# Kernel tuning notes

Measured on AMD Instinct MI355X. Metric: run time of the kernel, lower is better.

The kernel has to match this reference:

```python
import jax, jax.numpy as jnp
import numpy as np

K = 3
STRIDE = 1
PAD = 1
DIL = 1


def conv2d(x, w, b, stride, pad, dil):
    y = jax.lax.conv_general_dilated(
        x, w, (stride, stride), [(pad, pad), (pad, pad)],
        rhs_dilation=(dil, dil), dimension_numbers=("NCHW", "OIHW", "NCHW"))
    return y + b[None, :, None, None]


def bilinear_gather(img, ys, xs):
    # img: (C,H,W); ys,xs: (KK,Ho,Wo) pixel coords.
    # grid_sample(mode=bilinear, padding_mode=zeros, align_corners=True):
    # out-of-range corners contribute 0, interpolation weights unchanged.
    H, W = img.shape[-2:]
    y0 = jnp.floor(ys)
    x0 = jnp.floor(xs)
    wy1 = ys - y0
    wx1 = xs - x0
    wy0 = 1.0 - wy1
    wx0 = 1.0 - wx1

    def g(yc, xc):
        yi = yc.astype(jnp.int32)
        xi = xc.astype(jnp.int32)
        valid = (yi >= 0) & (yi < H) & (xi >= 0) & (xi < W)
        yi = jnp.clip(yi, 0, H - 1)
        xi = jnp.clip(xi, 0, W - 1)
        v = img[:, yi, xi]  # (C,KK,Ho,Wo)
        return v * valid[None].astype(img.dtype)

    return (g(y0, x0) * (wy0 * wx0)[None]
            + g(y0, x0 + 1.0) * (wy0 * wx1)[None]
            + g(y0 + 1.0, x0) * (wy1 * wx0)[None]
            + g(y0 + 1.0, x0 + 1.0) * (wy1 * wx1)[None])


def setup_inputs() -> dict:
    key = jax.random.key(0)
    ks = jax.random.split(key, 4)
    B, C_in, H, W = 8, 64, 96, 96
    C_out = 64
    x = jax.random.normal(ks[0], (B, C_in, H, W), dtype=jnp.float32)
    weight = jax.random.normal(ks[1], (C_out, C_in, K, K), dtype=jnp.float32) * 0.05
    bias = jax.random.normal(ks[2], (C_out,), dtype=jnp.float32) * 0.01
    off_w = jax.random.normal(ks[3], (2 * K * K, C_in, K, K), dtype=jnp.float32) * 0.05
    off_b = jnp.zeros((2 * K * K,), dtype=jnp.float32)
    return {"x": x, "weight": weight, "bias": bias, "off_w": off_w, "off_b": off_b}


def reference(x, weight, bias, off_w, off_b):
    B, C, H, W = x.shape
    Ho = (H + 2 * PAD - DIL * (K - 1) - 1) // STRIDE + 1
    Wo = (W + 2 * PAD - DIL * (K - 1) - 1) // STRIDE + 1

    offsets = conv2d(x, off_w, off_b, STRIDE, PAD, DIL)  # (B,2*K*K,Ho,Wo)
    off = offsets.reshape(B, K * K, 2, Ho, Wo)

    # Base sampling grid (note: original code does NOT subtract padding; kept faithful).
    by, bx = jnp.meshgrid(jnp.arange(Ho, dtype=x.dtype), jnp.arange(Wo, dtype=x.dtype), indexing="ij")
    by = by * STRIDE + (K // 2) * DIL
    bx = bx * STRIDE + (K // 2) * DIL
    ko = jnp.arange(-(K // 2), K // 2 + 1, dtype=x.dtype)
    ky, kx = jnp.meshgrid(ko, ko, indexing="ij")

    sy = by[None, None] + ky.reshape(1, -1, 1, 1) + off[:, :, 0]  # (B,KK,Ho,Wo)
    sx = bx[None, None] + kx.reshape(1, -1, 1, 1) + off[:, :, 1]

    sampled = jax.vmap(bilinear_gather)(x, sy, sx)  # (B,C,KK,Ho,Wo)

    wflat = weight.reshape(weight.shape[0], C, K * K)  # (O,C,KK)
    out = jnp.einsum("bckhw,ock->bohw", sampled, wflat)
    return out + bias[None, :, None, None]
```

## Files before the change

### kernel.cpp

```cpp
#include <hip/hip_runtime.h>

#define HH 96
#define WW 96
#define HW 9216
#define NB 8

typedef __bf16 bf16x8 __attribute__((ext_vector_type(8)));
typedef float  f32x4  __attribute__((ext_vector_type(4)));

union BF8 { uint4 u; bf16x8 v; unsigned short s[8]; };

__device__ __forceinline__ unsigned short f2bf_bits(float f) {
    unsigned u = __float_as_uint(f);
    unsigned r = u + 0x7FFFu + ((u >> 16) & 1u);
    return (unsigned short)(r >> 16);
}
__device__ __forceinline__ float bf2f(unsigned short s) {
    return __uint_as_float(((unsigned)s) << 16);
}

__device__ __forceinline__ void bl_setup(int h, int w, int r, int s, float oy, float ox,
                                         int* a, float* wg) {
    float sy = (float)(h + r) + oy;
    float sx = (float)(w + s) + ox;
    float fy = floorf(sy), fx = floorf(sx);
    int   y0 = (int)fy, x0 = (int)fx;
    int   y1 = y0 + 1, x1 = x0 + 1;
    float wy1 = sy - fy, wx1 = sx - fx;
    float wy0 = 1.f - wy1, wx0 = 1.f - wx1;
    float m00 = (y0 >= 0 && y0 < HH && x0 >= 0 && x0 < WW) ? 1.f : 0.f;
    float m01 = (y0 >= 0 && y0 < HH && x1 >= 0 && x1 < WW) ? 1.f : 0.f;
    float m10 = (y1 >= 0 && y1 < HH && x0 >= 0 && x0 < WW) ? 1.f : 0.f;
    float m11 = (y1 >= 0 && y1 < HH && x1 >= 0 && x1 < WW) ? 1.f : 0.f;
    int cy0 = min(max(y0, 0), HH - 1), cy1 = min(max(y1, 0), HH - 1);
    int cx0 = min(max(x0, 0), WW - 1), cx1 = min(max(x1, 0), WW - 1);
    a[0] = (cy0 * WW + cx0) * 64;  a[1] = (cy0 * WW + cx1) * 64;
    a[2] = (cy1 * WW + cx0) * 64;  a[3] = (cy1 * WW + cx1) * 64;
    wg[0] = wy0 * wx0 * m00;  wg[1] = wy0 * wx1 * m01;
    wg[2] = wy1 * wx0 * m10;  wg[3] = wy1 * wx1 * m11;
}

__global__ __launch_bounds__(256) void xcvt_prep(const float* __restrict__ x,
                                                 const float* __restrict__ weight,
                                                 const float* __restrict__ off_w,
                                                 unsigned short* __restrict__ xt,
                                                 unsigned short* __restrict__ wTb,
                                                 unsigned short* __restrict__ owTb) {
    __shared__ unsigned short T[64 * 64];
    int bid   = blockIdx.x;
    int t     = threadIdx.x;
    int b     = bid & 7;
    int pbase = (bid >> 3) * 64;
    int pl    = t & 63;
    int q     = t >> 6;

    const float* xp = x + ((size_t)(b * 64 + q * 16)) * HW + pbase + pl;
    unsigned short hb[16];
#pragma unroll
    for (int i = 0; i < 16; ++i) hb[i] = f2bf_bits(xp[(size_t)i * HW]);

    uint4 w0, w1;
    w0.x = hb[0]  | (hb[1]  << 16); w0.y = hb[2]  | (hb[3]  << 16);
    w0.z = hb[4]  | (hb[5]  << 16); w0.w = hb[6]  | (hb[7]  << 16);
    w1.x = hb[8]  | (hb[9]  << 16); w1.y = hb[10] | (hb[11] << 16);
    w1.z = hb[12] | (hb[13] << 16); w1.w = hb[14] | (hb[15] << 16);
    int sw = pl & 7;
    *(uint4*)&T[pl * 64 + (((2 * q)     ^ sw) << 3)] = w0;
    *(uint4*)&T[pl * 64 + (((2 * q + 1) ^ sw) << 3)] = w1;
    __syncthreads();

    int row = t >> 2, rs = row & 7;
    uint4 a  = *(const uint4*)&T[row * 64 + ((((t & 3) * 2)     ^ rs) << 3)];
    uint4 b2 = *(const uint4*)&T[row * 64 + ((((t & 3) * 2 + 1) ^ rs) << 3)];
    unsigned short* dst = xt + ((size_t)(b * HW + pbase)) * 64 + t * 16;
    *(uint4*)dst       = a;
    *(uint4*)(dst + 8) = b2;

    if (bid < 216) {
        int i = bid * 256 + t;
        if (i < 36864) {
            int tap = i >> 12;
            int co  = (i >> 6) & 63;
            int c   = i & 63;
            wTb[i] = f2bf_bits(weight[(co * 64 + c) * 9 + tap]);
        } else {
            int f   = i - 36864;
            int j   = f / 576;
            int kk  = f - j * 576;
            int tap = kk >> 6;
            int c   = kk & 63;
            owTb[f] = (j < 18) ? f2bf_bits(off_w[(j * 64 + c) * 9 + tap]) : (unsigned short)0;
        }
    }
}

__global__ __launch_bounds__(256) void offs_mfma(const unsigned short* __restrict__ xt,
                                                 const unsigned short* __restrict__ owTb,
                                                 const float* __restrict__ ob,
                                                 float* __restrict__ off) {
    __shared__ unsigned short S[64 * 64];

    int bid   = blockIdx.x;
    int t     = threadIdx.x;
    int b     = bid & 7;
    int pbase = (bid >> 3) * 64;

    int e    = t & 7;
    int base = t >> 3;
    int px0  = pbase + base;
    int px1  = px0 + 32;
    int h0 = px0 / WW, w0 = px0 - h0 * WW;
    int h1 = px1 / WW, w1 = px1 - h1 * WW;
    int sw = base & 7;

    int ln = t & 15;
    int qd = (t >> 4) & 3;
    int pt = t >> 6;

    f32x4 accj[2] = {{0.f, 0.f, 0.f, 0.f}, {0.f, 0.f, 0.f, 0.f}};
    const unsigned short* xb = xt + (size_t)b * HW * 64;

    for (int tap = 0; tap < 9; ++tap) {
        int r = tap / 3, s = tap - r * 3;

        int  iy0 = h0 - 1 + r, ix0 = w0 - 1 + s;
        bool v0  = (iy0 >= 0) & (iy0 < HH) & (ix0 >= 0) & (ix0 < WW);
        int  a0  = (min(max(iy0, 0), HH - 1) * WW + min(max(ix0, 0), WW - 1)) * 64;
        int  iy1 = h1 - 1 + r, ix1 = w1 - 1 + s;
        bool v1  = (iy1 >= 0) & (iy1 < HH) & (ix1 >= 0) & (ix1 < WW);
        int  a1  = (min(max(iy1, 0), HH - 1) * WW + min(max(ix1, 0), WW - 1)) * 64;

        uint4 p0 = *(const uint4*)(xb + a0 + e * 8);
        uint4 p1 = *(const uint4*)(xb + a1 + e * 8);
        if (!v0) p0 = make_uint4(0, 0, 0, 0);
        if (!v1) p1 = make_uint4(0, 0, 0, 0);
        *(uint4*)&S[base * 64 + ((e ^ sw) << 3)]        = p0;
        *(uint4*)&S[(base + 32) * 64 + ((e ^ sw) << 3)] = p1;
        __syncthreads();

        int  row = pt * 16 + ln, rs = row & 7;
        BF8  fa0, fa1;
        fa0.u = *(const uint4*)&S[row * 64 + ((qd       ^ rs) << 3)];
        fa1.u = *(const uint4*)&S[row * 64 + (((qd + 4) ^ rs) << 3)];
#pragma unroll
        for (int jt = 0; jt < 2; ++jt) {
            const unsigned short* brow = owTb + (size_t)(jt * 16 + ln) * 576 + tap * 64 + qd * 8;
            BF8 fb0, fb1;
            fb0.u = *(const uint4*)brow;
            fb1.u = *(const uint4*)(brow + 32);
            accj[jt] = __builtin_amdgcn_mfma_f32_16x16x32_bf16(fa0.v, fb0.v, accj[jt], 0, 0, 0);
            accj[jt] = __builtin_amdgcn_mfma_f32_16x16x32_bf16(fa1.v, fb1.v, accj[jt], 0, 0, 0);
        }
        __syncthreads();
    }

    int pxo = pbase + pt * 16 + qd * 4;
    {
        float bv = ob[ln];
        float4 st;
        st.x = accj[0].x + bv; st.y = accj[0].y + bv;
        st.z = accj[0].z + bv; st.w = accj[0].w + bv;
        *(float4*)(off + ((size_t)(b * 18 + ln)) * HW + pxo) = st;
    }
    if (ln < 2) {
        int   j  = 16 + ln;
        float bv = ob[j];
        float4 st;
        st.x = accj[1].x + bv; st.y = accj[1].y + bv;
        st.z = accj[1].z + bv; st.w = accj[1].w + bv;
        *(float4*)(off + ((size_t)(b * 18 + j)) * HW + pxo) = st;
    }
}

__global__ __launch_bounds__(256) void deform_main(const unsigned short* __restrict__ xt,
                                                   const unsigned short* __restrict__ wTb,
                                                   const float* __restrict__ bias,
                                                   const float* __restrict__ off,
                                                   float* __restrict__ out) {
    __shared__ unsigned short S[64 * 64];
    __shared__ unsigned short Wk[64 * 64];

    int bid   = blockIdx.x;
    int t     = threadIdx.x;
    int b     = bid & 7;
    int pbase = (bid >> 3) * 64;

    int e    = t & 7;
    int base = t >> 3;
    int px0  = pbase + base;
    int px1  = px0 + 32;
    int h0 = px0 / WW, w0 = px0 - h0 * WW;
    int h1 = px1 / WW, w1 = px1 - h1 * WW;
    int sw = base & 7;

    int ln = t & 15;
    int qd = (t >> 4) & 3;
    int ct = t >> 6;

    const unsigned short* xb = xt + (size_t)b * HW * 64;
    const float* offb = off + (size_t)b * 18 * HW;

    f32x4 acc[4] = {{0.f,0.f,0.f,0.f},{0.f,0.f,0.f,0.f},{0.f,0.f,0.f,0.f},{0.f,0.f,0.f,0.f}};

    float oy0 = offb[0 * HW + px0], ox0 = offb[1 * HW + px0];
    float oy1 = offb[0 * HW + px1], ox1 = offb[1 * HW + px1];

    for (int tap = 0; tap < 9; ++tap) {
        int r = tap / 3, s = tap - r * 3;

        int   a0[4], a1[4];
        float g0[4], g1[4];
        bl_setup(h0, w0, r, s, oy0, ox0, a0, g0);
        bl_setup(h1, w1, r, s, oy1, ox1, a1, g1);

        uint4 cA[4], cB[4];
#pragma unroll
        for (int c = 0; c < 4; ++c) cA[c] = *(const uint4*)(xb + a0[c] + e * 8);
#pragma unroll
        for (int c = 0; c < 4; ++c) cB[c] = *(const uint4*)(xb + a1[c] + e * 8);

        float oy0N = 0.f, ox0N = 0.f, oy1N = 0.f, ox1N = 0.f;
        if (tap < 8) {
            oy0N = offb[(2 * tap + 2) * HW + px0]; ox0N = offb[(2 * tap + 3) * HW + px0];
            oy1N = offb[(2 * tap + 2) * HW + px1]; ox1N = offb[(2 * tap + 3) * HW + px1];
        }

        {
            const uint4* wsrc = (const uint4*)(wTb + (size_t)tap * 4096);
            uint4 wa = wsrc[2 * t];
            uint4 wb = wsrc[2 * t + 1];
            int co = t >> 2, cs = co & 7;
            int c0 = (t & 3) * 2;
            *(uint4*)&Wk[co * 64 + ((c0       ^ cs) << 3)] = wa;
            *(uint4*)&Wk[co * 64 + (((c0 + 1) ^ cs) << 3)] = wb;
        }

        {
            BF8 q0, q1, q2, q3;
            q0.u = cA[0]; q1.u = cA[1]; q2.u = cA[2]; q3.u = cA[3];
            unsigned short ov[8];
#pragma unroll
            for (int i = 0; i < 8; ++i) {
                float v = g0[0] * bf2f(q0.s[i]) + g0[1] * bf2f(q1.s[i])
                        + g0[2] * bf2f(q2.s[i]) + g0[3] * bf2f(q3.s[i]);
                ov[i] = f2bf_bits(v);
            }
            uint4 sv;
            sv.x = ov[0] | (ov[1] << 16); sv.y = ov[2] | (ov[3] << 16);
            sv.z = ov[4] | (ov[5] << 16); sv.w = ov[6] | (ov[7] << 16);
            *(uint4*)&S[base * 64 + ((e ^ sw) << 3)] = sv;
        }
        {
            BF8 q0, q1, q2, q3;
            q0.u = cB[0]; q1.u = cB[1]; q2.u = cB[2]; q3.u = cB[3];
            unsigned short ov[8];
#pragma unroll
            for (int i = 0; i < 8; ++i) {
                float v = g1[0] * bf2f(q0.s[i]) + g1[1] * bf2f(q1.s[i])
                        + g1[2] * bf2f(q2.s[i]) + g1[3] * bf2f(q3.s[i]);
                ov[i] = f2bf_bits(v);
            }
            uint4 sv;
            sv.x = ov[0] | (ov[1] << 16); sv.y = ov[2] | (ov[3] << 16);
            sv.z = ov[4] | (ov[5] << 16); sv.w = ov[6] | (ov[7] << 16);
            *(uint4*)&S[(base + 32) * 64 + ((e ^ sw) << 3)] = sv;
        }
        __syncthreads();

        {
            int  wrow = ct * 16 + ln, ws2 = wrow & 7;
            BF8  fb0, fb1;
            fb0.u = *(const uint4*)&Wk[wrow * 64 + ((qd       ^ ws2) << 3)];
            fb1.u = *(const uint4*)&Wk[wrow * 64 + (((qd + 4) ^ ws2) << 3)];
#pragma unroll
            for (int pt = 0; pt < 4; ++pt) {
                int row = pt * 16 + ln, rs = row & 7;
                BF8 fa0, fa1;
                fa0.u = *(const uint4*)&S[row * 64 + ((qd       ^ rs) << 3)];
                fa1.u = *(const uint4*)&S[row * 64 + (((qd + 4) ^ rs) << 3)];
                acc[pt] = __builtin_amdgcn_mfma_f32_16x16x32_bf16(fa0.v, fb0.v, acc[pt], 0, 0, 0);
                acc[pt] = __builtin_amdgcn_mfma_f32_16x16x32_bf16(fa1.v, fb1.v, acc[pt], 0, 0, 0);
            }
        }
        __syncthreads();

        oy0 = oy0N; ox0 = ox0N; oy1 = oy1N; ox1 = ox1N;
    }

    int   co = ct * 16 + ln;
    float bv = bias[co];
    float* ob2 = out + ((size_t)(b * 64 + co)) * HW + pbase + qd * 4;
#pragma unroll
    for (int pt = 0; pt < 4; ++pt) {
        float4 st;
        st.x = acc[pt].x + bv; st.y = acc[pt].y + bv;
        st.z = acc[pt].z + bv; st.w = acc[pt].w + bv;
        *(float4*)(ob2 + pt * 16) = st;
    }
}

extern "C" void kernel_launch(void* const* d_in, const int* in_sizes, int n_in,
                              void* d_out, int out_size, void* d_ws, size_t ws_size,
                              hipStream_t stream) {
    const float* x      = (const float*)d_in[0];
    const float* weight = (const float*)d_in[1];
    const float* bias   = (const float*)d_in[2];
    const float* off_w  = (const float*)d_in[3];
    const float* off_b  = (const float*)d_in[4];
    float* out = (float*)d_out;

    float*          offbuf = (float*)d_ws;
    unsigned short* xt     = (unsigned short*)(offbuf + 1327104);
    unsigned short* wTb    = xt + 4718592;
    unsigned short* owTb   = wTb + 36864;

    hipLaunchKernelGGL(xcvt_prep,   dim3(1152), dim3(256), 0, stream,
                       x, weight, off_w, xt, wTb, owTb);
    hipLaunchKernelGGL(offs_mfma,   dim3(1152), dim3(256), 0, stream,
                       xt, owTb, off_b, offbuf);
    hipLaunchKernelGGL(deform_main, dim3(1152), dim3(256), 0, stream,
                       xt, wTb, bias, offbuf, out);
}
```

Measured before the change: 136.4 us.

## Fuse offset conv into deformable conv kernel and keep offsets in LDS

Merges the offset-convolution kernel into the main deformable-conv kernel so each block computes its 64 pixels' offsets with MFMA, stores them in shared memory and uses them directly for bilinear sampling. This removes one kernel launch and the global write and read of the offset buffer. It also double-buffers the shared sample tile to drop one barrier per tap, reads the weight fragments straight from global memory instead of staging them in LDS, and uses the packed bf16 conversion intrinsic. The trade-offs are more LDS per block and weight loads that now go through cache rather than shared memory.

```diff
diff --git a/kernel.cpp b/kernel.cpp
--- a/kernel.cpp
+++ b/kernel.cpp
@@ -1,4 +1,5 @@
 #include <hip/hip_runtime.h>
+#include <hip/hip_bf16.h>
 
 #define HH 96
 #define WW 96
@@ -17,6 +18,11 @@
 }
 __device__ __forceinline__ float bf2f(unsigned short s) {
     return __uint_as_float(((unsigned)s) << 16);
+}
+__device__ __forceinline__ unsigned pkbf(float a, float b) {
+    union { __hip_bfloat162 h; unsigned u; } c;
+    c.h = __float22bfloat162_rn(make_float2(a, b));
+    return c.u;
 }
 
 __device__ __forceinline__ void bl_setup(int h, int w, int r, int s, float oy, float ox,
@@ -94,11 +100,14 @@
     }
 }
 
-__global__ __launch_bounds__(256) void offs_mfma(const unsigned short* __restrict__ xt,
-                                                 const unsigned short* __restrict__ owTb,
-                                                 const float* __restrict__ ob,
-                                                 float* __restrict__ off) {
-    __shared__ unsigned short S[64 * 64];
+__global__ __launch_bounds__(256) void deform_all(const unsigned short* __restrict__ xt,
+                                                  const unsigned short* __restrict__ wTb,
+                                                  const unsigned short* __restrict__ owTb,
+                                                  const float* __restrict__ bias,
+                                                  const float* __restrict__ ob,
+                                                  float* __restrict__ out) {
+    __shared__ unsigned short S[2][64 * 64];
+    __shared__ float offs[64 * 20];
 
     int bid   = blockIdx.x;
     int t     = threadIdx.x;
@@ -115,12 +124,14 @@
 
     int ln = t & 15;
     int qd = (t >> 4) & 3;
-    int pt = t >> 6;
+    int wv = t >> 6;
+
+    const unsigned short* xb = xt + (size_t)b * HW * 64;
 
     f32x4 accj[2] = {{0.f, 0.f, 0.f, 0.f}, {0.f, 0.f, 0.f, 0.f}};
-    const unsigned short* xb = xt + (size_t)b * HW * 64;
 
     for (int tap = 0; tap < 9; ++tap) {
+        int cur = tap & 1;
         int r = tap / 3, s = tap - r * 3;
 
         int  iy0 = h0 - 1 + r, ix0 = w0 - 1 + s;
@@ -134,14 +145,14 @@
         uint4 p1 = *(const uint4*)(xb + a1 + e * 8);
         if (!v0) p0 = make_uint4(0, 0, 0, 0);
         if (!v1) p1 = make_uint4(0, 0, 0, 0);
-        *(uint4*)&S[base * 64 + ((e ^ sw) << 3)]        = p0;
-        *(uint4*)&S[(base + 32) * 64 + ((e ^ sw) << 3)] = p1;
+        *(uint4*)&S[cur][base * 64 + ((e ^ sw) << 3)]        = p0;
+        *(uint4*)&S[cur][(base + 32) * 64 + ((e ^ sw) << 3)] = p1;
         __syncthreads();
 
-        int  row = pt * 16 + ln, rs = row & 7;
+        int  row = wv * 16 + ln, rs = row & 7;
         BF8  fa0, fa1;
-        fa0.u = *(const uint4*)&S[row * 64 + ((qd       ^ rs) << 3)];
-        fa1.u = *(const uint4*)&S[row * 64 + (((qd + 4) ^ rs) << 3)];
+        fa0.u = *(const uint4*)&S[cur][row * 64 + ((qd       ^ rs) << 3)];
+        fa1.u = *(const uint4*)&S[cur][row * 64 + (((qd + 4) ^ rs) << 3)];
 #pragma unroll
         for (int jt = 0; jt < 2; ++jt) {
             const unsigned short* brow = owTb + (size_t)(jt * 16 + ln) * 576 + tap * 64 + qd * 8;
@@ -151,62 +162,29 @@
             accj[jt] = __builtin_amdgcn_mfma_f32_16x16x32_bf16(fa0.v, fb0.v, accj[jt], 0, 0, 0);
             accj[jt] = __builtin_amdgcn_mfma_f32_16x16x32_bf16(fa1.v, fb1.v, accj[jt], 0, 0, 0);
         }
-        __syncthreads();
-    }
-
-    int pxo = pbase + pt * 16 + qd * 4;
+    }
+
     {
-        float bv = ob[ln];
-        float4 st;
-        st.x = accj[0].x + bv; st.y = accj[0].y + bv;
-        st.z = accj[0].z + bv; st.w = accj[0].w + bv;
-        *(float4*)(off + ((size_t)(b * 18 + ln)) * HW + pxo) = st;
-    }
-    if (ln < 2) {
-        int   j  = 16 + ln;
-        float bv = ob[j];
-        float4 st;
-        st.x = accj[1].x + bv; st.y = accj[1].y + bv;
-        st.z = accj[1].z + bv; st.w = accj[1].w + bv;
-        *(float4*)(off + ((size_t)(b * 18 + j)) * HW + pxo) = st;
-    }
-}
-
-__global__ __launch_bounds__(256) void deform_main(const unsigned short* __restrict__ xt,
-                                                   const unsigned short* __restrict__ wTb,
-                                                   const float* __restrict__ bias,
-                                                   const float* __restrict__ off,
-                                                   float* __restrict__ out) {
-    __shared__ unsigned short S[64 * 64];
-    __shared__ unsigned short Wk[64 * 64];
-
-    int bid   = blockIdx.x;
-    int t     = threadIdx.x;
-    int b     = bid & 7;
-    int pbase = (bid >> 3) * 64;
-
-    int e    = t & 7;
-    int base = t >> 3;
-    int px0  = pbase + base;
-    int px1  = px0 + 32;
-    int h0 = px0 / WW, w0 = px0 - h0 * WW;
-    int h1 = px1 / WW, w1 = px1 - h1 * WW;
-    int sw = base & 7;
-
-    int ln = t & 15;
-    int qd = (t >> 4) & 3;
-    int ct = t >> 6;
-
-    const unsigned short* xb = xt + (size_t)b * HW * 64;
-    const float* offb = off + (size_t)b * 18 * HW;
+        int   rowp = wv * 16 + qd * 4;
+        float obj = ob[ln];
+#pragma unroll
+        for (int rg = 0; rg < 4; ++rg) offs[(rowp + rg) * 20 + ln] = accj[0][rg] + obj;
+        if (ln < 2) {
+            float obj1 = ob[16 + ln];
+#pragma unroll
+            for (int rg = 0; rg < 4; ++rg) offs[(rowp + rg) * 20 + 16 + ln] = accj[1][rg] + obj1;
+        }
+    }
+    __syncthreads();
 
     f32x4 acc[4] = {{0.f,0.f,0.f,0.f},{0.f,0.f,0.f,0.f},{0.f,0.f,0.f,0.f},{0.f,0.f,0.f,0.f}};
 
-    float oy0 = offb[0 * HW + px0], ox0 = offb[1 * HW + px0];
-    float oy1 = offb[0 * HW + px1], ox1 = offb[1 * HW + px1];
-
     for (int tap = 0; tap < 9; ++tap) {
+        int cur = tap & 1;
         int r = tap / 3, s = tap - r * 3;
+
+        float oy0 = offs[base * 20 + 2 * tap],        ox0 = offs[base * 20 + 2 * tap + 1];
+        float oy1 = offs[(base + 32) * 20 + 2 * tap], ox1 = offs[(base + 32) * 20 + 2 * tap + 1];
 
         int   a0[4], a1[4];
         float g0[4], g1[4];
@@ -219,75 +197,52 @@
 #pragma unroll
         for (int c = 0; c < 4; ++c) cB[c] = *(const uint4*)(xb + a1[c] + e * 8);
 
-        float oy0N = 0.f, ox0N = 0.f, oy1N = 0.f, ox1N = 0.f;
-        if (tap < 8) {
-            oy0N = offb[(2 * tap + 2) * HW + px0]; ox0N = offb[(2 * tap + 3) * HW + px0];
-            oy1N = offb[(2 * tap + 2) * HW + px1]; ox1N = offb[(2 * tap + 3) * HW + px1];
-        }
-
-        {
-            const uint4* wsrc = (const uint4*)(wTb + (size_t)tap * 4096);
-            uint4 wa = wsrc[2 * t];
-            uint4 wb = wsrc[2 * t + 1];
-            int co = t >> 2, cs = co & 7;
-            int c0 = (t & 3) * 2;
-            *(uint4*)&Wk[co * 64 + ((c0       ^ cs) << 3)] = wa;
-            *(uint4*)&Wk[co * 64 + (((c0 + 1) ^ cs) << 3)] = wb;
-        }
-
         {
             BF8 q0, q1, q2, q3;
             q0.u = cA[0]; q1.u = cA[1]; q2.u = cA[2]; q3.u = cA[3];
-            unsigned short ov[8];
-#pragma unroll
-            for (int i = 0; i < 8; ++i) {
-                float v = g0[0] * bf2f(q0.s[i]) + g0[1] * bf2f(q1.s[i])
-                        + g0[2] * bf2f(q2.s[i]) + g0[3] * bf2f(q3.s[i]);
-                ov[i] = f2bf_bits(v);
-            }
+            float v[8];
+#pragma unroll
+            for (int i = 0; i < 8; ++i)
+                v[i] = g0[0] * bf2f(q0.s[i]) + g0[1] * bf2f(q1.s[i])
+                     + g0[2] * bf2f(q2.s[i]) + g0[3] * bf2f(q3.s[i]);
             uint4 sv;
-            sv.x = ov[0] | (ov[1] << 16); sv.y = ov[2] | (ov[3] << 16);
-            sv.z = ov[4] | (ov[5] << 16); sv.w = ov[6] | (ov[7] << 16);
-            *(uint4*)&S[base * 64 + ((e ^ sw) << 3)] = sv;
+            sv.x = pkbf(v[0], v[1]); sv.y = pkbf(v[2], v[3]);
+            sv.z = pkbf(v[4], v[5]); sv.w = pkbf(v[6], v[7]);
+            *(uint4*)&S[cur][base * 64 + ((e ^ sw) << 3)] = sv;
         }
         {
             BF8 q0, q1, q2, q3;
             q0.u = cB[0]; q1.u = cB[1]; q2.u = cB[2]; q3.u = cB[3];
-            unsigned short ov[8];
-#pragma unroll
-            for (int i = 0; i < 8; ++i) {
-                float v = g1[0] * bf2f(q0.s[i]) + g1[1] * bf2f(q1.s[i])
-                        + g1[2] * bf2f(q2.s[i]) + g1[3] * bf2f(q3.s[i]);
-                ov[i] = f2bf_bits(v);
-            }
+            float v[8];
+#pragma unroll
+            for (int i = 0; i < 8; ++i)
+                v[i] = g1[0] * bf2f(q0.s[i]) + g1[1] * bf2f(q1.s[i])
+                     + g1[2] * bf2f(q2.s[i]) + g1[3] * bf2f(q3.s[i]);
             uint4 sv;
-            sv.x = ov[0] | (ov[1] << 16); sv.y = ov[2] | (ov[3] << 16);
-            sv.z = ov[4] | (ov[5] << 16); sv.w = ov[6] | (ov[7] << 16);
-            *(uint4*)&S[(base + 32) * 64 + ((e ^ sw) << 3)] = sv;
+            sv.x = pkbf(v[0], v[1]); sv.y = pkbf(v[2], v[3]);
+            sv.z = pkbf(v[4], v[5]); sv.w = pkbf(v[6], v[7]);
+            *(uint4*)&S[cur][(base + 32) * 64 + ((e ^ sw) << 3)] = sv;
         }
         __syncthreads();
 
         {
-            int  wrow = ct * 16 + ln, ws2 = wrow & 7;
-            BF8  fb0, fb1;
-            fb0.u = *(const uint4*)&Wk[wrow * 64 + ((qd       ^ ws2) << 3)];
-            fb1.u = *(const uint4*)&Wk[wrow * 64 + (((qd + 4) ^ ws2) << 3)];
+            const unsigned short* wb = wTb + (size_t)tap * 4096 + (wv * 16 + ln) * 64 + qd * 8;
+            BF8 fb0, fb1;
+            fb0.u = *(const uint4*)wb;
+            fb1.u = *(const uint4*)(wb + 32);
 #pragma unroll
             for (int pt = 0; pt < 4; ++pt) {
                 int row = pt * 16 + ln, rs = row & 7;
                 BF8 fa0, fa1;
-                fa0.u = *(const uint4*)&S[row * 64 + ((qd       ^ rs) << 3)];
-                fa1.u = *(const uint4*)&S[row * 64 + (((qd + 4) ^ rs) << 3)];
+                fa0.u = *(const uint4*)&S[cur][row * 64 + ((qd       ^ rs) << 3)];
+                fa1.u = *(const uint4*)&S[cur][row * 64 + (((qd + 4) ^ rs) << 3)];
                 acc[pt] = __builtin_amdgcn_mfma_f32_16x16x32_bf16(fa0.v, fb0.v, acc[pt], 0, 0, 0);
                 acc[pt] = __builtin_amdgcn_mfma_f32_16x16x32_bf16(fa1.v, fb1.v, acc[pt], 0, 0, 0);
             }
         }
-        __syncthreads();
-
-        oy0 = oy0N; ox0 = ox0N; oy1 = oy1N; ox1 = ox1N;
-    }
-
-    int   co = ct * 16 + ln;
+    }
+
+    int   co = wv * 16 + ln;
     float bv = bias[co];
     float* ob2 = out + ((size_t)(b * 64 + co)) * HW + pbase + qd * 4;
 #pragma unroll
@@ -309,15 +264,12 @@
     const float* off_b  = (const float*)d_in[4];
     float* out = (float*)d_out;
 
-    float*          offbuf = (float*)d_ws;
-    unsigned short* xt     = (unsigned short*)(offbuf + 1327104);
-    unsigned short* wTb    = xt + 4718592;
-    unsigned short* owTb   = wTb + 36864;
-
-    hipLaunchKernelGGL(xcvt_prep,   dim3(1152), dim3(256), 0, stream,
+    unsigned short* xt   = (unsigned short*)d_ws;
+    unsigned short* wTb  = xt + 4718592;
+    unsigned short* owTb = wTb + 36864;
+
+    hipLaunchKernelGGL(xcvt_prep,  dim3(1152), dim3(256), 0, stream,
                        x, weight, off_w, xt, wTb, owTb);
-    hipLaunchKernelGGL(offs_mfma,   dim3(1152), dim3(256), 0, stream,
-                       xt, owTb, off_b, offbuf);
-    hipLaunchKernelGGL(deform_main, dim3(1152), dim3(256), 0, stream,
-                       xt, wTb, bias, offbuf, out);
-}
+    hipLaunchKernelGGL(deform_all, dim3(1152), dim3(256), 0, stream,
+                       xt, wTb, owTb, bias, off_b, out);
+}
```

Result: faster. 132.5 us (-2.9%).
